# Optimization experiments

Hardware: AMD Instinct MI355X
Metric: run time of the kernel (lower is better)

Reference implementation:

```python
import jax, jax.numpy as jnp
import numpy as np

N, E, H, NH = 50000, 800000, 64, 4
DK = H // NH
EPS_LN = 1e-5


def _layernorm(h, g, b):
    mu = jnp.mean(h, axis=-1, keepdims=True)
    var = jnp.mean((h - mu) ** 2, axis=-1, keepdims=True)
    return (h - mu) * jax.lax.rsqrt(var + EPS_LN) * g + b


def _mlp(h, w0, b0, w1, b1, w2, b2, g, be):
    # Linear -> ReLU -> Linear -> ReLU -> Linear -> LayerNorm (mlp_layers=2)
    h = jax.nn.relu(h @ w0.T + b0)
    h = jax.nn.relu(h @ w1.T + b1)
    h = h @ w2.T + b2
    return _layernorm(h, g, be)


def setup_inputs() -> dict:
    key = jax.random.key(0)
    ks = jax.random.split(key, 24)
    s = lambda i, shape: jax.random.normal(ks[i], shape, jnp.float32) * (1.0 / np.sqrt(shape[-1]))
    inp = {
        "x": jax.random.normal(ks[0], (N, H), jnp.float32),
        "edge_index": jax.random.randint(ks[1], (2, E), 0, N),
        "edge_attr": jax.random.normal(ks[2], (E, H), jnp.float32),
        # edge MLP: Linear(3H,H), Linear(H,H), Linear(H,H), LayerNorm(H)
        "e_w0": s(3, (H, 3 * H)), "e_b0": jnp.zeros((H,)),
        "e_w1": s(4, (H, H)),     "e_b1": jnp.zeros((H,)),
        "e_w2": s(5, (H, H)),     "e_b2": jnp.zeros((H,)),
        "e_g": jnp.ones((H,)),    "e_be": jnp.zeros((H,)),
        # node MLP: Linear(2H,H), Linear(H,H), Linear(H,H), LayerNorm(H)
        "n_w0": s(6, (H, 2 * H)), "n_b0": jnp.zeros((H,)),
        "n_w1": s(7, (H, H)),     "n_b1": jnp.zeros((H,)),
        "n_w2": s(8, (H, H)),     "n_b2": jnp.zeros((H,)),
        "n_g": jnp.ones((H,)),    "n_be": jnp.zeros((H,)),
        "wq": s(9, (H, H)), "wk": s(10, (H, H)), "wv": s(11, (H, H)), "wo": s(12, (H, H)),
    }
    return inp


def reference(x, edge_index, edge_attr,
              e_w0, e_b0, e_w1, e_b1, e_w2, e_b2, e_g, e_be,
              n_w0, n_b0, n_w1, n_b1, n_w2, n_b2, n_g, n_be,
              wq, wk, wv, wo):
    src, dst = edge_index[0], edge_index[1]
    n_nodes, hid = x.shape
    n_edges = src.shape[0]
    x_dst, x_src = x[dst], x[src]  # [E,H] gathers

    e_new = _mlp(jnp.concatenate([x_dst, x_src, edge_attr], axis=-1),
                 e_w0, e_b0, e_w1, e_b1, e_w2, e_b2, e_g, e_be)

    Q = (x_dst @ wq.T).reshape(n_edges, NH, DK)
    K = (x_src @ wk.T).reshape(n_edges, NH, DK)
    V = (e_new @ wv.T).reshape(n_edges, NH, DK)

    scores = jnp.sum(Q * K, axis=-1) / np.sqrt(DK)  # [E,NH]
    smax = jax.ops.segment_max(scores, dst, num_segments=n_nodes)  # [N,NH]
    exp_s = jnp.exp(scores - smax[dst])
    sum_exp = jax.ops.segment_sum(exp_s, dst, num_segments=n_nodes)
    alpha = exp_s / (sum_exp[dst] + 1e-12)  # [E,NH]

    msg = jax.ops.segment_sum((alpha[..., None] * V).reshape(n_edges, hid),
                              dst, num_segments=n_nodes)  # [N,H]
    msg = msg @ wo.T

    x_new = x + _mlp(jnp.concatenate([x, msg], axis=-1),
                     n_w0, n_b0, n_w1, n_b1, n_w2, n_b2, n_g, n_be)
    return (x_new, edge_attr + e_new)
```

## Files before the change

kernel.cpp:

```cpp
#include <hip/hip_runtime.h>

typedef __bf16 bf16;
typedef __attribute__((ext_vector_type(8))) __bf16 bf16x8;
typedef __attribute__((ext_vector_type(4))) __bf16 bf16x4;
typedef __attribute__((ext_vector_type(4))) float  f32x4;

__device__ __forceinline__ f32x4 mfma16(bf16x8 a, bf16x8 b, f32x4 c) {
    return __builtin_amdgcn_mfma_f32_16x16x32_bf16(a, b, c, 0, 0, 0);
}

__device__ __forceinline__ void stash8(bf16* dst, float4 a, float4 b) {
    bf16x8 v;
    v[0] = (bf16)a.x; v[1] = (bf16)a.y; v[2] = (bf16)a.z; v[3] = (bf16)a.w;
    v[4] = (bf16)b.x; v[5] = (bf16)b.y; v[6] = (bf16)b.z; v[7] = (bf16)b.w;
    *reinterpret_cast<bf16x8*>(dst) = v;
}

__device__ __forceinline__ bf16x8 wfrag(const bf16* __restrict__ W, int s, int n, int lane) {
    return *reinterpret_cast<const bf16x8*>(W + (((s * 4 + n) * 64 + lane) * 8));
}

template<int P, int KS>
__device__ __forceinline__ void mm2s(const bf16* __restrict__ src, int kofs,
                                     const bf16* __restrict__ W,
                                     int lane, f32x4 (&acc)[2][4]) {
    const int c16 = lane & 15, g = lane >> 4;
#pragma unroll
    for (int m = 0; m < 2; ++m)
#pragma unroll
        for (int n = 0; n < 4; ++n) acc[m][n] = 0.0f;
#pragma unroll
    for (int s = 0; s < KS; ++s) {
        bf16x8 aA = *reinterpret_cast<const bf16x8*>(src + c16 * P + kofs + s * 32 + g * 8);
        bf16x8 aB = *reinterpret_cast<const bf16x8*>(src + (16 + c16) * P + kofs + s * 32 + g * 8);
#pragma unroll
        for (int n = 0; n < 4; ++n) {
            bf16x8 bb = wfrag(W, s, n, lane);
            acc[0][n] = mfma16(aA, bb, acc[0][n]);
            acc[1][n] = mfma16(aB, bb, acc[1][n]);
        }
    }
}

template<int P, int KS>
__device__ __forceinline__ void mm1s(const bf16* __restrict__ src, int kofs,
                                     const bf16* __restrict__ W,
                                     int lane, f32x4 (&acc)[4]) {
    const int c16 = lane & 15, g = lane >> 4;
#pragma unroll
    for (int n = 0; n < 4; ++n) acc[n] = 0.0f;
#pragma unroll
    for (int s = 0; s < KS; ++s) {
        bf16x8 a = *reinterpret_cast<const bf16x8*>(src + c16 * P + kofs + s * 32 + g * 8);
#pragma unroll
        for (int n = 0; n < 4; ++n) {
            bf16x8 bb = wfrag(W, s, n, lane);
            acc[n] = mfma16(a, bb, acc[n]);
        }
    }
}

__device__ __forceinline__ void storeh2(bf16* hbw, const f32x4 (&acc)[2][4],
                                        const float* __restrict__ bias, int c16, int g) {
#pragma unroll
    for (int n = 0; n < 4; ++n) {
        float bb = bias[n * 16 + c16];
#pragma unroll
        for (int m = 0; m < 2; ++m)
#pragma unroll
            for (int r = 0; r < 4; ++r)
                hbw[(m * 16 + g * 4 + r) * 72 + n * 16 + c16] = (bf16)fmaxf(acc[m][n][r] + bb, 0.0f);
    }
}

__device__ __forceinline__ void storeh1(bf16* hbw, const f32x4 (&acc)[4],
                                        const float* __restrict__ bias, int c16, int g) {
#pragma unroll
    for (int n = 0; n < 4; ++n) {
        float bb = bias[n * 16 + c16];
#pragma unroll
        for (int r = 0; r < 4; ++r)
            hbw[(g * 4 + r) * 72 + n * 16 + c16] = (bf16)fmaxf(acc[n][r] + bb, 0.0f);
    }
}

struct PrepArgs {
    const float* src[10];
    bf16* dst[10];
    int ofs[11];
    int ldk[10];
};

__global__ void prep_kernel(PrepArgs a, int totalFrag) {
    int t = blockIdx.x * 256 + threadIdx.x;
    if (t >= totalFrag) return;
    int eb = t * 8;
    int k = 0;
    while (k < 9 && eb >= a.ofs[k + 1]) ++k;
    int f = (eb - a.ofs[k]) >> 3;
    int lane = f & 63, n = (f >> 6) & 3, s = f >> 8;
    int c16 = lane & 15, g = lane >> 4;
    const float* sp = a.src[k] + (n * 16 + c16) * a.ldk[k] + s * 32 + g * 8;
    float4 v0 = *reinterpret_cast<const float4*>(sp);
    float4 v1 = *reinterpret_cast<const float4*>(sp + 4);
    stash8(a.dst[k] + (size_t)f * 8, v0, v1);
}

__global__ __launch_bounds__(256) void xb_kernel(const float* __restrict__ x,
                                                 bf16* __restrict__ xb, int total8) {
    int t = blockIdx.x * 256 + threadIdx.x;
    if (t >= total8) return;
    const float4* p = reinterpret_cast<const float4*>(x) + t * 2;
    stash8(xb + (size_t)t * 8, p[0], p[1]);
}

__global__ __launch_bounds__(256) void degcnt_kernel(const int* __restrict__ ei,
                                                     int* __restrict__ deg, int E) {
    int e = blockIdx.x * 256 + threadIdx.x;
    if (e < E) atomicAdd(&deg[ei[E + e]], 1);
}

__global__ __launch_bounds__(256) void scan1_kernel(const int* __restrict__ deg, int* __restrict__ ofs,
                                                    int* __restrict__ bsum, int N) {
    __shared__ int ws4[4];
    const int t = threadIdx.x, lane = t & 63, w = t >> 6;
    const int i = blockIdx.x * 256 + t;
    const int v = (i < N) ? deg[i] : 0;
    int inc = v;
#pragma unroll
    for (int o = 1; o < 64; o <<= 1) { int u = __shfl_up(inc, o); if (lane >= o) inc += u; }
    if (lane == 63) ws4[w] = inc;
    __syncthreads();
    int add = 0;
    for (int k = 0; k < w; ++k) add += ws4[k];
    if (i < N) ofs[i] = inc - v + add;
    if (t == 255) bsum[blockIdx.x] = inc + add;
}

__global__ __launch_bounds__(256) void scan2_kernel(int* __restrict__ bsum, int nb) {
    __shared__ int ws4[4];
    const int t = threadIdx.x, lane = t & 63, w = t >> 6;
    const int v = (t < nb) ? bsum[t] : 0;
    int inc = v;
#pragma unroll
    for (int o = 1; o < 64; o <<= 1) { int u = __shfl_up(inc, o); if (lane >= o) inc += u; }
    if (lane == 63) ws4[w] = inc;
    __syncthreads();
    int add = 0;
    for (int k = 0; k < w; ++k) add += ws4[k];
    if (t < nb) bsum[t] = inc - v + add;
}

__global__ __launch_bounds__(256) void scan3_kernel(int* __restrict__ ofs, const int* __restrict__ bsum, int N) {
    const int i = blockIdx.x * 256 + threadIdx.x;
    if (i < N) ofs[i] += bsum[blockIdx.x];
}

__global__ __launch_bounds__(256) void fill_kernel(const int* __restrict__ ei, const int* __restrict__ ofs,
                                                   int* __restrict__ cur, int* __restrict__ eidT, int E) {
    const int e = blockIdx.x * 256 + threadIdx.x;
    if (e >= E) return;
    const int d = ei[E + e];
    const int slot = atomicAdd(&cur[d], 1);
    eidT[ofs[d] + slot] = e;
}

__global__ __launch_bounds__(256, 4) void e1_kernel(
    const bf16* __restrict__ xb, const int* __restrict__ ei, const float* __restrict__ ea,
    const bf16* __restrict__ W0, const bf16* __restrict__ W1, const bf16* __restrict__ W2,
    const bf16* __restrict__ Wq, const bf16* __restrict__ Wk, const bf16* __restrict__ Wv,
    const float* __restrict__ b0, const float* __restrict__ b1, const float* __restrict__ b2,
    const float* __restrict__ egm, const float* __restrict__ ebe,
    float* __restrict__ scoresOut, bf16* __restrict__ Vout, float* __restrict__ eout, int E)
{
    __shared__ bf16 eas[4][32][72];
    __shared__ bf16 hbl[4][32][72];
    const int w = threadIdx.x >> 6;
    const int lane = threadIdx.x & 63;
    const int ebase = blockIdx.x * 128 + w * 32;
    bf16* eaw = &eas[w][0][0];
    bf16* hbw = &hbl[w][0][0];
    const int g = lane >> 4, c16 = lane & 15;

    {
        const int rr = lane >> 4;
        const int cc = (lane & 15) * 4;
#pragma unroll
        for (int i = 0; i < 8; ++i) {
            int row = i * 4 + rr;
            float4 v = *reinterpret_cast<const float4*>(ea + (size_t)(ebase + row) * 64 + cc);
            bf16x4 o;
            o[0] = (bf16)v.x; o[1] = (bf16)v.y; o[2] = (bf16)v.z; o[3] = (bf16)v.w;
            *reinterpret_cast<bf16x4*>(eaw + row * 72 + cc) = o;
        }
    }

    const int eA0 = ebase + c16, eA1 = ebase + 16 + c16;
    const int dn0 = ei[E + eA0], dn1 = ei[E + eA1];
    const int sn0 = ei[eA0],     sn1 = ei[eA1];
    const bf16* xd0 = xb + (size_t)dn0 * 64;
    const bf16* xd1 = xb + (size_t)dn1 * 64;
    const bf16* xs0 = xb + (size_t)sn0 * 64;
    const bf16* xs1 = xb + (size_t)sn1 * 64;
    bf16x8 fxd[2][2], fxs[2][2];
#pragma unroll
    for (int s = 0; s < 2; ++s) {
        fxd[0][s] = *reinterpret_cast<const bf16x8*>(xd0 + s * 32 + g * 8);
        fxd[1][s] = *reinterpret_cast<const bf16x8*>(xd1 + s * 32 + g * 8);
        fxs[0][s] = *reinterpret_cast<const bf16x8*>(xs0 + s * 32 + g * 8);
        fxs[1][s] = *reinterpret_cast<const bf16x8*>(xs1 + s * 32 + g * 8);
    }

    {
        f32x4 aq[2][4], ak[2][4];
#pragma unroll
        for (int m = 0; m < 2; ++m)
#pragma unroll
            for (int n = 0; n < 4; ++n) { aq[m][n] = 0.0f; ak[m][n] = 0.0f; }
#pragma unroll
        for (int s = 0; s < 2; ++s)
#pragma unroll
            for (int n = 0; n < 4; ++n) {
                bf16x8 bq = wfrag(Wq, s, n, lane);
                bf16x8 bk = wfrag(Wk, s, n, lane);
                aq[0][n] = mfma16(fxd[0][s], bq, aq[0][n]);
                aq[1][n] = mfma16(fxd[1][s], bq, aq[1][n]);
                ak[0][n] = mfma16(fxs[0][s], bk, ak[0][n]);
                ak[1][n] = mfma16(fxs[1][s], bk, ak[1][n]);
            }
        float* sst = reinterpret_cast<float*>(hbw);
#pragma unroll
        for (int n = 0; n < 4; ++n) {
#pragma unroll
            for (int m = 0; m < 2; ++m) {
                float pr[4];
#pragma unroll
                for (int r = 0; r < 4; ++r) pr[r] = aq[m][n][r] * ak[m][n][r];
#pragma unroll
                for (int ms = 1; ms < 16; ms <<= 1)
#pragma unroll
                    for (int r = 0; r < 4; ++r) pr[r] += __shfl_xor(pr[r], ms);
                if (c16 == n) {
#pragma unroll
                    for (int r = 0; r < 4; ++r)
                        sst[(m * 16 + g * 4 + r) * 4 + n] = pr[r] * 0.25f;
                }
            }
        }
        float2 sv = *reinterpret_cast<const float2*>(sst + lane * 2);
        *reinterpret_cast<float2*>(scoresOut + (size_t)ebase * 4 + lane * 2) = sv;
    }

    f32x4 acc[2][4], acc2[2][4];
#pragma unroll
    for (int m = 0; m < 2; ++m)
#pragma unroll
        for (int n = 0; n < 4; ++n) acc[m][n] = 0.0f;
#pragma unroll
    for (int s = 0; s < 2; ++s)
#pragma unroll
        for (int n = 0; n < 4; ++n) {
            bf16x8 bd = wfrag(W0, s, n, lane);
            acc[0][n] = mfma16(fxd[0][s], bd, acc[0][n]);
            acc[1][n] = mfma16(fxd[1][s], bd, acc[1][n]);
            bf16x8 bs = wfrag(W0, s + 2, n, lane);
            acc[0][n] = mfma16(fxs[0][s], bs, acc[0][n]);
            acc[1][n] = mfma16(fxs[1][s], bs, acc[1][n]);
        }
#pragma unroll
    for (int s = 0; s < 2; ++s) {
        bf16x8 ae0 = *reinterpret_cast<const bf16x8*>(eaw + c16 * 72 + s * 32 + g * 8);
        bf16x8 ae1 = *reinterpret_cast<const bf16x8*>(eaw + (16 + c16) * 72 + s * 32 + g * 8);
#pragma unroll
        for (int n = 0; n < 4; ++n) {
            bf16x8 be = wfrag(W0, s + 4, n, lane);
            acc[0][n] = mfma16(ae0, be, acc[0][n]);
            acc[1][n] = mfma16(ae1, be, acc[1][n]);
        }
    }

    storeh2(hbw, acc, b0, c16, g);
    mm2s<72, 2>(hbw, 0, W1, lane, acc);
    storeh2(hbw, acc, b1, c16, g);
    mm2s<72, 2>(hbw, 0, W2, lane, acc2);
#pragma unroll
    for (int n = 0; n < 4; ++n) {
        float bb = b2[n * 16 + c16];
#pragma unroll
        for (int m = 0; m < 2; ++m)
#pragma unroll
            for (int r = 0; r < 4; ++r) acc2[m][n][r] += bb;
    }

    float mu[2][4], rs[2][4];
#pragma unroll
    for (int m = 0; m < 2; ++m)
#pragma unroll
        for (int r = 0; r < 4; ++r) {
            float s1 = acc2[m][0][r] + acc2[m][1][r] + acc2[m][2][r] + acc2[m][3][r];
            for (int ms = 1; ms < 16; ms <<= 1) s1 += __shfl_xor(s1, ms);
            float mm = s1 * (1.0f / 64.0f);
            float d0 = acc2[m][0][r] - mm, d1 = acc2[m][1][r] - mm;
            float d2 = acc2[m][2][r] - mm, d3 = acc2[m][3][r] - mm;
            float sq = d0 * d0 + d1 * d1 + d2 * d2 + d3 * d3;
            for (int ms = 1; ms < 16; ms <<= 1) sq += __shfl_xor(sq, ms);
            mu[m][r] = mm;
            rs[m][r] = rsqrtf(sq * (1.0f / 64.0f) + 1e-5f);
        }

#pragma unroll
    for (int n = 0; n < 4; ++n) {
        float gg = egm[n * 16 + c16], bb = ebe[n * 16 + c16];
#pragma unroll
        for (int m = 0; m < 2; ++m)
#pragma unroll
            for (int r = 0; r < 4; ++r) {
                int rowi = m * 16 + g * 4 + r;
                float v = (acc2[m][n][r] - mu[m][r]) * rs[m][r] * gg + bb;
                hbw[rowi * 72 + n * 16 + c16] = (bf16)v;
            }
    }

    {
        const int rr = lane >> 4;
        const int cc = (lane & 15) * 4;
#pragma unroll
        for (int i = 0; i < 8; ++i) {
            int row = i * 4 + rr;
            bf16x4 hv = *reinterpret_cast<const bf16x4*>(hbw + row * 72 + cc);
            bf16x4 av = *reinterpret_cast<const bf16x4*>(eaw + row * 72 + cc);
            float4 o;
            o.x = (float)av[0] + (float)hv[0];
            o.y = (float)av[1] + (float)hv[1];
            o.z = (float)av[2] + (float)hv[2];
            o.w = (float)av[3] + (float)hv[3];
            *reinterpret_cast<float4*>(eout + (size_t)(ebase + row) * 64 + cc) = o;
        }
    }

    mm2s<72, 2>(hbw, 0, Wv, lane, acc);
#pragma unroll
    for (int n = 0; n < 4; ++n)
#pragma unroll
        for (int m = 0; m < 2; ++m)
#pragma unroll
            for (int r = 0; r < 4; ++r)
                eaw[(m * 16 + g * 4 + r) * 72 + n * 16 + c16] = (bf16)acc[m][n][r];
#pragma unroll
    for (int k = 0; k < 4; ++k) {
        int row = k * 8 + (lane >> 3);
        int col = (lane & 7) * 8;
        bf16x8 v = *reinterpret_cast<const bf16x8*>(eaw + row * 72 + col);
        *reinterpret_cast<bf16x8*>(Vout + (size_t)(ebase + row) * 64 + col) = v;
    }
}

__global__ __launch_bounds__(256) void gather_kernel(
    const int* __restrict__ deg, const int* __restrict__ ofs, const int* __restrict__ eidT,
    const float* __restrict__ scores, const bf16* __restrict__ V,
    bf16* __restrict__ msg, int N)
{
    const int w = threadIdx.x >> 6, lane = threadIdx.x & 63;
    const int n = blockIdx.x * 4 + w;
    if (n >= N) return;
    const int cnt = deg[n];
    const int* lst = eidT + ofs[n];
    const int h = lane >> 4;
    float m = -3.4e38f, s = 0.f, acc = 0.f;

    int eA = (lane < cnt) ? lst[lane] : 0;
    int eB = (64 + lane < cnt) ? lst[64 + lane] : 0;
    const int nr = min(cnt, 128);
    if (nr > 0) {
        int e = __shfl(eA, 0);
        float sc = scores[(size_t)e * 4 + h];
        float v  = (float)V[(size_t)e * 64 + lane];
        for (int i = 1; i <= nr; ++i) {
            float sc2 = 0.f, v2 = 0.f;
            if (i < nr) {
                int e2 = __shfl((i < 64) ? eA : eB, i & 63);
                sc2 = scores[(size_t)e2 * 4 + h];
                v2  = (float)V[(size_t)e2 * 64 + lane];
            }
            float mn = fmaxf(m, sc);
            float c  = __expf(m - mn);
            float ex = __expf(sc - mn);
            s = s * c + ex;
            acc = acc * c + ex * v;
            m = mn;
            sc = sc2; v = v2;
        }
    }
    for (int i = 128; i < cnt; ++i) {
        int e = lst[i];
        float sc = scores[(size_t)e * 4 + h];
        float v  = (float)V[(size_t)e * 64 + lane];
        float mn = fmaxf(m, sc);
        float c  = __expf(m - mn);
        float ex = __expf(sc - mn);
        s = s * c + ex;
        acc = acc * c + ex * v;
        m = mn;
    }
    msg[(size_t)n * 64 + lane] = (bf16)(acc / (s + 1e-12f));
}

__global__ __launch_bounds__(256, 4) void n_kernel(
    const float* __restrict__ x, const bf16* __restrict__ msg,
    const bf16* __restrict__ Wo, const bf16* __restrict__ W0, const bf16* __restrict__ W1,
    const bf16* __restrict__ W2,
    const float* __restrict__ b0, const float* __restrict__ b1, const float* __restrict__ b2,
    const float* __restrict__ ngm, const float* __restrict__ nbe,
    float* __restrict__ xout, int N)
{
    __shared__ bf16 cat[4][16][136];
    __shared__ bf16 hbl[4][16][72];
    const int w = threadIdx.x >> 6, lane = threadIdx.x & 63;
    const int nbase = blockIdx.x * 64 + w * 16;
    bf16* catw = &cat[w][0][0];
    bf16* hbw  = &hbl[w][0][0];

    {
        const int r = lane >> 2, q = lane & 3;
        const int nd = min(nbase + r, N - 1);
        const float4* xp = reinterpret_cast<const float4*>(x) + (size_t)nd * 16 + q * 4;
        stash8(catw + r * 136 + q * 16,     xp[0], xp[1]);
        stash8(catw + r * 136 + q * 16 + 8, xp[2], xp[3]);
        const bf16* mp = msg + (size_t)nd * 64 + q * 16;
        *reinterpret_cast<bf16x8*>(hbw + r * 72 + q * 16)     = *reinterpret_cast<const bf16x8*>(mp);
        *reinterpret_cast<bf16x8*>(hbw + r * 72 + q * 16 + 8) = *reinterpret_cast<const bf16x8*>(mp + 8);
    }
    const int g = lane >> 4, c16 = lane & 15;
    f32x4 acc[4];

    mm1s<72, 2>(hbw, 0, Wo, lane, acc);
#pragma unroll
    for (int n = 0; n < 4; ++n)
#pragma unroll
        for (int r = 0; r < 4; ++r)
            catw[(g * 4 + r) * 136 + 64 + n * 16 + c16] = (bf16)acc[n][r];

    mm1s<136, 4>(catw, 0, W0, lane, acc);
    storeh1(hbw, acc, b0, c16, g);
    mm1s<72, 2>(hbw, 0, W1, lane, acc);
    storeh1(hbw, acc, b1, c16, g);
    mm1s<72, 2>(hbw, 0, W2, lane, acc);
#pragma unroll
    for (int n = 0; n < 4; ++n) {
        float bb = b2[n * 16 + c16];
#pragma unroll
        for (int r = 0; r < 4; ++r) acc[n][r] += bb;
    }

    float mu[4], rs[4];
#pragma unroll
    for (int r = 0; r < 4; ++r) {
        float s1 = acc[0][r] + acc[1][r] + acc[2][r] + acc[3][r];
        for (int ms = 1; ms < 16; ms <<= 1) s1 += __shfl_xor(s1, ms);
        float mm = s1 * (1.0f / 64.0f);
        float d0 = acc[0][r] - mm, d1 = acc[1][r] - mm, d2 = acc[2][r] - mm, d3 = acc[3][r] - mm;
        float sq = d0 * d0 + d1 * d1 + d2 * d2 + d3 * d3;
        for (int ms = 1; ms < 16; ms <<= 1) sq += __shfl_xor(sq, ms);
        mu[r] = mm;
        rs[r] = rsqrtf(sq * (1.0f / 64.0f) + 1e-5f);
    }
#pragma unroll
    for (int n = 0; n < 4; ++n) {
        float gg = ngm[n * 16 + c16], bb = nbe[n * 16 + c16];
#pragma unroll
        for (int r = 0; r < 4; ++r) {
            int rowi = g * 4 + r;
            int node = nbase + rowi;
            float v = (acc[n][r] - mu[r]) * rs[r] * gg + bb;
            if (node < N) {
                size_t o = (size_t)node * 64 + n * 16 + c16;
                xout[o] = x[o] + v;
            }
        }
    }
}

extern "C" void kernel_launch(void* const* d_in, const int* in_sizes, int n_in,
                              void* d_out, int out_size, void* d_ws, size_t ws_size,
                              hipStream_t stream)
{
    const float* x   = (const float*)d_in[0];
    const int*   ei  = (const int*)d_in[1];
    const float* ea  = (const float*)d_in[2];
    const float* ew0 = (const float*)d_in[3];
    const float* eb0 = (const float*)d_in[4];
    const float* ew1 = (const float*)d_in[5];
    const float* eb1 = (const float*)d_in[6];
    const float* ew2 = (const float*)d_in[7];
    const float* eb2 = (const float*)d_in[8];
    const float* egm = (const float*)d_in[9];
    const float* ebe = (const float*)d_in[10];
    const float* nw0 = (const float*)d_in[11];
    const float* nb0 = (const float*)d_in[12];
    const float* nw1 = (const float*)d_in[13];
    const float* nb1 = (const float*)d_in[14];
    const float* nw2 = (const float*)d_in[15];
    const float* nb2 = (const float*)d_in[16];
    const float* ngm = (const float*)d_in[17];
    const float* nbe = (const float*)d_in[18];
    const float* wq  = (const float*)d_in[19];
    const float* wk  = (const float*)d_in[20];
    const float* wv  = (const float*)d_in[21];
    const float* wo  = (const float*)d_in[22];

    const int Nn = in_sizes[0] / 64;
    const int Ee = in_sizes[1] / 2;

    char* p = (char*)d_ws;
    auto carve = [&](size_t bytes) {
        char* r = p;
        p += (bytes + 255) & ~(size_t)255;
        return r;
    };
    bf16* W0e = (bf16*)carve(64 * 192 * 2);
    bf16* W1e = (bf16*)carve(64 * 64 * 2);
    bf16* W2e = (bf16*)carve(64 * 64 * 2);
    bf16* Wqb = (bf16*)carve(64 * 64 * 2);
    bf16* Wkb = (bf16*)carve(64 * 64 * 2);
    bf16* Wvb = (bf16*)carve(64 * 64 * 2);
    bf16* Wob = (bf16*)carve(64 * 64 * 2);
    bf16* W0n = (bf16*)carve(64 * 128 * 2);
    bf16* W1n = (bf16*)carve(64 * 64 * 2);
    bf16* W2n = (bf16*)carve(64 * 64 * 2);
    float* scores = (float*)carve((size_t)Ee * 4 * 4);
    bf16*  V      = (bf16*)carve((size_t)Ee * 64 * 2);
    bf16*  msg    = (bf16*)carve((size_t)Nn * 64 * 2);
    bf16*  xb     = (bf16*)carve((size_t)Nn * 64 * 2);
    int*   deg    = (int*)carve((size_t)Nn * 4);
    int*   ofs    = (int*)carve((size_t)Nn * 4);
    int*   cur    = (int*)carve((size_t)Nn * 4);
    int*   eidT   = (int*)carve((size_t)Ee * 4);
    int*   bsum   = (int*)carve(((size_t)Nn / 256 + 2) * 4);

    hipMemsetAsync(deg, 0, (size_t)Nn * 4, stream);
    hipMemsetAsync(cur, 0, (size_t)Nn * 4, stream);

    PrepArgs pa;
    const float* srcs[10] = {ew0, ew1, ew2, wq, wk, wv, wo, nw0, nw1, nw2};
    bf16* dsts[10]        = {W0e, W1e, W2e, Wqb, Wkb, Wvb, Wob, W0n, W1n, W2n};
    const int sizes[10]   = {12288, 4096, 4096, 4096, 4096, 4096, 4096, 8192, 4096, 4096};
    const int ldks[10]    = {192, 64, 64, 64, 64, 64, 64, 128, 64, 64};
    int acc_ofs = 0;
    for (int i = 0; i < 10; ++i) {
        pa.src[i] = srcs[i];
        pa.dst[i] = dsts[i];
        pa.ofs[i] = acc_ofs;
        pa.ldk[i] = ldks[i];
        acc_ofs += sizes[i];
    }
    pa.ofs[10] = acc_ofs;
    const int totalFrag = acc_ofs / 8;
    prep_kernel<<<(totalFrag + 255) / 256, 256, 0, stream>>>(pa, totalFrag);

    const int total8 = Nn * 64 / 8;
    xb_kernel<<<(total8 + 255) / 256, 256, 0, stream>>>(x, xb, total8);

    degcnt_kernel<<<(Ee + 255) / 256, 256, 0, stream>>>(ei, deg, Ee);
    const int nb = (Nn + 255) / 256;
    scan1_kernel<<<nb, 256, 0, stream>>>(deg, ofs, bsum, Nn);
    scan2_kernel<<<1, 256, 0, stream>>>(bsum, nb);
    scan3_kernel<<<nb, 256, 0, stream>>>(ofs, bsum, Nn);
    fill_kernel<<<(Ee + 255) / 256, 256, 0, stream>>>(ei, ofs, cur, eidT, Ee);

    float* xout = (float*)d_out;
    float* eout = (float*)d_out + (size_t)Nn * 64;

    e1_kernel<<<Ee / 128, 256, 0, stream>>>(xb, ei, ea,
                                            W0e, W1e, W2e, Wqb, Wkb, Wvb,
                                            eb0, eb1, eb2, egm, ebe,
                                            scores, V, eout, Ee);

    gather_kernel<<<(Nn + 3) / 4, 256, 0, stream>>>(deg, ofs, eidT, scores, V, msg, Nn);

    n_kernel<<<(Nn + 63) / 64, 256, 0, stream>>>(x, msg, Wob, W0n, W1n, W2n,
                                                 nb0, nb1, nb2, ngm, nbe, xout, Nn);
}
```

Measured before the change: 416.2 us.

## Loop e1 kernel over multiple tiles with software-prefetched gathers; fuse setup kernels

The edge kernel now processes five 128-edge tiles per block. While the current tile is computed, it prefetches the next tile's edge_attr, its edge indices and the gathered x rows into registers, to hide global gather latency behind the MFMA work. Launch bounds drop from 4 to 3 waves per SIMD to leave room for the extra registers, at some cost in occupancy. Separately, the weight prep, x-to-bf16 and degree-count kernels are merged into one launch to cut launch overhead.

```diff
diff --git a/kernel.cpp b/kernel.cpp
--- a/kernel.cpp
+++ b/kernel.cpp
@@ -91,33 +91,33 @@
     int ldk[10];
 };
 
-__global__ void prep_kernel(PrepArgs a, int totalFrag) {
+__global__ __launch_bounds__(256) void setup_kernel(PrepArgs a, int totalFrag,
+                                                    const float* __restrict__ x,
+                                                    bf16* __restrict__ xbuf, int total8,
+                                                    const int* __restrict__ ei,
+                                                    int* __restrict__ deg, int E) {
     int t = blockIdx.x * 256 + threadIdx.x;
-    if (t >= totalFrag) return;
-    int eb = t * 8;
-    int k = 0;
-    while (k < 9 && eb >= a.ofs[k + 1]) ++k;
-    int f = (eb - a.ofs[k]) >> 3;
-    int lane = f & 63, n = (f >> 6) & 3, s = f >> 8;
-    int c16 = lane & 15, g = lane >> 4;
-    const float* sp = a.src[k] + (n * 16 + c16) * a.ldk[k] + s * 32 + g * 8;
-    float4 v0 = *reinterpret_cast<const float4*>(sp);
-    float4 v1 = *reinterpret_cast<const float4*>(sp + 4);
-    stash8(a.dst[k] + (size_t)f * 8, v0, v1);
-}
-
-__global__ __launch_bounds__(256) void xb_kernel(const float* __restrict__ x,
-                                                 bf16* __restrict__ xb, int total8) {
-    int t = blockIdx.x * 256 + threadIdx.x;
-    if (t >= total8) return;
-    const float4* p = reinterpret_cast<const float4*>(x) + t * 2;
-    stash8(xb + (size_t)t * 8, p[0], p[1]);
-}
-
-__global__ __launch_bounds__(256) void degcnt_kernel(const int* __restrict__ ei,
-                                                     int* __restrict__ deg, int E) {
-    int e = blockIdx.x * 256 + threadIdx.x;
-    if (e < E) atomicAdd(&deg[ei[E + e]], 1);
+    if (t < totalFrag) {
+        int eb = t * 8;
+        int k = 0;
+        while (k < 9 && eb >= a.ofs[k + 1]) ++k;
+        int f = (eb - a.ofs[k]) >> 3;
+        int lane = f & 63, n = (f >> 6) & 3, s = f >> 8;
+        int c16 = lane & 15, g = lane >> 4;
+        const float* sp = a.src[k] + (n * 16 + c16) * a.ldk[k] + s * 32 + g * 8;
+        float4 v0 = *reinterpret_cast<const float4*>(sp);
+        float4 v1 = *reinterpret_cast<const float4*>(sp + 4);
+        stash8(a.dst[k] + (size_t)f * 8, v0, v1);
+        return;
+    }
+    t -= totalFrag;
+    if (t < total8) {
+        const float4* p = reinterpret_cast<const float4*>(x) + t * 2;
+        stash8(xbuf + (size_t)t * 8, p[0], p[1]);
+        return;
+    }
+    t -= total8;
+    if (t < E) atomicAdd(&deg[ei[E + t]], 1);
 }
 
 __global__ __launch_bounds__(256) void scan1_kernel(const int* __restrict__ deg, int* __restrict__ ofs,
@@ -165,165 +165,187 @@
     eidT[ofs[d] + slot] = e;
 }
 
-__global__ __launch_bounds__(256, 4) void e1_kernel(
+template<int T>
+__global__ __launch_bounds__(256, 3) void e1_kernel(
     const bf16* __restrict__ xb, const int* __restrict__ ei, const float* __restrict__ ea,
     const bf16* __restrict__ W0, const bf16* __restrict__ W1, const bf16* __restrict__ W2,
     const bf16* __restrict__ Wq, const bf16* __restrict__ Wk, const bf16* __restrict__ Wv,
     const float* __restrict__ b0, const float* __restrict__ b1, const float* __restrict__ b2,
     const float* __restrict__ egm, const float* __restrict__ ebe,
-    float* __restrict__ scoresOut, bf16* __restrict__ Vout, float* __restrict__ eout, int E)
+    float* __restrict__ scoresOut, bf16* __restrict__ Vout, float* __restrict__ eout,
+    int tileOfs, int E)
 {
     __shared__ bf16 eas[4][32][72];
     __shared__ bf16 hbl[4][32][72];
     const int w = threadIdx.x >> 6;
     const int lane = threadIdx.x & 63;
-    const int ebase = blockIdx.x * 128 + w * 32;
+    const int g = lane >> 4, c16 = lane & 15;
+    const int rr = lane >> 4, cc = (lane & 15) * 4;
     bf16* eaw = &eas[w][0][0];
     bf16* hbw = &hbl[w][0][0];
-    const int g = lane >> 4, c16 = lane & 15;
-
+    const int tile0 = tileOfs + blockIdx.x * T;
+
+    float4 eaP[8];
+    int dn0, dn1, sn0, sn1;
     {
-        const int rr = lane >> 4;
-        const int cc = (lane & 15) * 4;
+        const int tb = tile0 * 128 + w * 32;
+#pragma unroll
+        for (int i = 0; i < 8; ++i)
+            eaP[i] = *reinterpret_cast<const float4*>(ea + (size_t)(tb + i * 4 + rr) * 64 + cc);
+        dn0 = ei[E + tb + c16]; dn1 = ei[E + tb + 16 + c16];
+        sn0 = ei[tb + c16];     sn1 = ei[tb + 16 + c16];
+    }
+    bf16x8 fxd[2][2], fxs[2][2];
+#pragma unroll
+    for (int s = 0; s < 2; ++s) {
+        fxd[0][s] = *reinterpret_cast<const bf16x8*>(xb + (size_t)dn0 * 64 + s * 32 + g * 8);
+        fxd[1][s] = *reinterpret_cast<const bf16x8*>(xb + (size_t)dn1 * 64 + s * 32 + g * 8);
+        fxs[0][s] = *reinterpret_cast<const bf16x8*>(xb + (size_t)sn0 * 64 + s * 32 + g * 8);
+        fxs[1][s] = *reinterpret_cast<const bf16x8*>(xb + (size_t)sn1 * 64 + s * 32 + g * 8);
+    }
+
+    for (int k = 0; k < T; ++k) {
+        const int ebase = (tile0 + k) * 128 + w * 32;
+
 #pragma unroll
         for (int i = 0; i < 8; ++i) {
-            int row = i * 4 + rr;
-            float4 v = *reinterpret_cast<const float4*>(ea + (size_t)(ebase + row) * 64 + cc);
             bf16x4 o;
-            o[0] = (bf16)v.x; o[1] = (bf16)v.y; o[2] = (bf16)v.z; o[3] = (bf16)v.w;
-            *reinterpret_cast<bf16x4*>(eaw + row * 72 + cc) = o;
-        }
-    }
-
-    const int eA0 = ebase + c16, eA1 = ebase + 16 + c16;
-    const int dn0 = ei[E + eA0], dn1 = ei[E + eA1];
-    const int sn0 = ei[eA0],     sn1 = ei[eA1];
-    const bf16* xd0 = xb + (size_t)dn0 * 64;
-    const bf16* xd1 = xb + (size_t)dn1 * 64;
-    const bf16* xs0 = xb + (size_t)sn0 * 64;
-    const bf16* xs1 = xb + (size_t)sn1 * 64;
-    bf16x8 fxd[2][2], fxs[2][2];
-#pragma unroll
-    for (int s = 0; s < 2; ++s) {
-        fxd[0][s] = *reinterpret_cast<const bf16x8*>(xd0 + s * 32 + g * 8);
-        fxd[1][s] = *reinterpret_cast<const bf16x8*>(xd1 + s * 32 + g * 8);
-        fxs[0][s] = *reinterpret_cast<const bf16x8*>(xs0 + s * 32 + g * 8);
-        fxs[1][s] = *reinterpret_cast<const bf16x8*>(xs1 + s * 32 + g * 8);
-    }
-
-    {
-        f32x4 aq[2][4], ak[2][4];
+            o[0] = (bf16)eaP[i].x; o[1] = (bf16)eaP[i].y;
+            o[2] = (bf16)eaP[i].z; o[3] = (bf16)eaP[i].w;
+            *reinterpret_cast<bf16x4*>(eaw + (i * 4 + rr) * 72 + cc) = o;
+        }
+
+        int ndn0, ndn1, nsn0, nsn1;
+        if (k + 1 < T) {
+            const int nb = ebase + 128;
+#pragma unroll
+            for (int i = 0; i < 8; ++i)
+                eaP[i] = *reinterpret_cast<const float4*>(ea + (size_t)(nb + i * 4 + rr) * 64 + cc);
+            ndn0 = ei[E + nb + c16]; ndn1 = ei[E + nb + 16 + c16];
+            nsn0 = ei[nb + c16];     nsn1 = ei[nb + 16 + c16];
+        }
+
+        {
+            f32x4 aq[2][4], ak[2][4];
+#pragma unroll
+            for (int m = 0; m < 2; ++m)
+#pragma unroll
+                for (int n = 0; n < 4; ++n) { aq[m][n] = 0.0f; ak[m][n] = 0.0f; }
+#pragma unroll
+            for (int s = 0; s < 2; ++s)
+#pragma unroll
+                for (int n = 0; n < 4; ++n) {
+                    bf16x8 bq = wfrag(Wq, s, n, lane);
+                    bf16x8 bk = wfrag(Wk, s, n, lane);
+                    aq[0][n] = mfma16(fxd[0][s], bq, aq[0][n]);
+                    aq[1][n] = mfma16(fxd[1][s], bq, aq[1][n]);
+                    ak[0][n] = mfma16(fxs[0][s], bk, ak[0][n]);
+                    ak[1][n] = mfma16(fxs[1][s], bk, ak[1][n]);
+                }
+            float* sst = reinterpret_cast<float*>(hbw);
+#pragma unroll
+            for (int n = 0; n < 4; ++n) {
+#pragma unroll
+                for (int m = 0; m < 2; ++m) {
+                    float pr[4];
+#pragma unroll
+                    for (int r = 0; r < 4; ++r) pr[r] = aq[m][n][r] * ak[m][n][r];
+#pragma unroll
+                    for (int ms = 1; ms < 16; ms <<= 1)
+#pragma unroll
+                        for (int r = 0; r < 4; ++r) pr[r] += __shfl_xor(pr[r], ms);
+                    if (c16 == n) {
+#pragma unroll
+                        for (int r = 0; r < 4; ++r)
+                            sst[(m * 16 + g * 4 + r) * 4 + n] = pr[r] * 0.25f;
+                    }
+                }
+            }
+            float2 sv = *reinterpret_cast<const float2*>(sst + lane * 2);
+            *reinterpret_cast<float2*>(scoresOut + (size_t)ebase * 4 + lane * 2) = sv;
+        }
+
+        f32x4 acc[2][4], acc2[2][4];
 #pragma unroll
         for (int m = 0; m < 2; ++m)
 #pragma unroll
-            for (int n = 0; n < 4; ++n) { aq[m][n] = 0.0f; ak[m][n] = 0.0f; }
+            for (int n = 0; n < 4; ++n) acc[m][n] = 0.0f;
 #pragma unroll
         for (int s = 0; s < 2; ++s)
 #pragma unroll
             for (int n = 0; n < 4; ++n) {
-                bf16x8 bq = wfrag(Wq, s, n, lane);
-                bf16x8 bk = wfrag(Wk, s, n, lane);
-                aq[0][n] = mfma16(fxd[0][s], bq, aq[0][n]);
-                aq[1][n] = mfma16(fxd[1][s], bq, aq[1][n]);
-                ak[0][n] = mfma16(fxs[0][s], bk, ak[0][n]);
-                ak[1][n] = mfma16(fxs[1][s], bk, ak[1][n]);
-            }
-        float* sst = reinterpret_cast<float*>(hbw);
+                bf16x8 bd = wfrag(W0, s, n, lane);
+                acc[0][n] = mfma16(fxd[0][s], bd, acc[0][n]);
+                acc[1][n] = mfma16(fxd[1][s], bd, acc[1][n]);
+                bf16x8 bs = wfrag(W0, s + 2, n, lane);
+                acc[0][n] = mfma16(fxs[0][s], bs, acc[0][n]);
+                acc[1][n] = mfma16(fxs[1][s], bs, acc[1][n]);
+            }
+#pragma unroll
+        for (int s = 0; s < 2; ++s) {
+            bf16x8 ae0 = *reinterpret_cast<const bf16x8*>(eaw + c16 * 72 + s * 32 + g * 8);
+            bf16x8 ae1 = *reinterpret_cast<const bf16x8*>(eaw + (16 + c16) * 72 + s * 32 + g * 8);
+#pragma unroll
+            for (int n = 0; n < 4; ++n) {
+                bf16x8 be = wfrag(W0, s + 4, n, lane);
+                acc[0][n] = mfma16(ae0, be, acc[0][n]);
+                acc[1][n] = mfma16(ae1, be, acc[1][n]);
+            }
+        }
+
+        bf16x8 nfxd[2][2], nfxs[2][2];
+        if (k + 1 < T) {
+#pragma unroll
+            for (int s = 0; s < 2; ++s) {
+                nfxd[0][s] = *reinterpret_cast<const bf16x8*>(xb + (size_t)ndn0 * 64 + s * 32 + g * 8);
+                nfxd[1][s] = *reinterpret_cast<const bf16x8*>(xb + (size_t)ndn1 * 64 + s * 32 + g * 8);
+                nfxs[0][s] = *reinterpret_cast<const bf16x8*>(xb + (size_t)nsn0 * 64 + s * 32 + g * 8);
+                nfxs[1][s] = *reinterpret_cast<const bf16x8*>(xb + (size_t)nsn1 * 64 + s * 32 + g * 8);
+            }
+        }
+
+        storeh2(hbw, acc, b0, c16, g);
+        mm2s<72, 2>(hbw, 0, W1, lane, acc);
+        storeh2(hbw, acc, b1, c16, g);
+        mm2s<72, 2>(hbw, 0, W2, lane, acc2);
 #pragma unroll
         for (int n = 0; n < 4; ++n) {
-#pragma unroll
-            for (int m = 0; m < 2; ++m) {
-                float pr[4];
-#pragma unroll
-                for (int r = 0; r < 4; ++r) pr[r] = aq[m][n][r] * ak[m][n][r];
-#pragma unroll
-                for (int ms = 1; ms < 16; ms <<= 1)
-#pragma unroll
-                    for (int r = 0; r < 4; ++r) pr[r] += __shfl_xor(pr[r], ms);
-                if (c16 == n) {
-#pragma unroll
-                    for (int r = 0; r < 4; ++r)
-                        sst[(m * 16 + g * 4 + r) * 4 + n] = pr[r] * 0.25f;
+            float bb = b2[n * 16 + c16];
+#pragma unroll
+            for (int m = 0; m < 2; ++m)
+#pragma unroll
+                for (int r = 0; r < 4; ++r) acc2[m][n][r] += bb;
+        }
+
+        float mu[2][4], rs[2][4];
+#pragma unroll
+        for (int m = 0; m < 2; ++m)
+#pragma unroll
+            for (int r = 0; r < 4; ++r) {
+                float s1 = acc2[m][0][r] + acc2[m][1][r] + acc2[m][2][r] + acc2[m][3][r];
+                for (int ms = 1; ms < 16; ms <<= 1) s1 += __shfl_xor(s1, ms);
+                float mm = s1 * (1.0f / 64.0f);
+                float d0 = acc2[m][0][r] - mm, d1 = acc2[m][1][r] - mm;
+                float d2 = acc2[m][2][r] - mm, d3 = acc2[m][3][r] - mm;
+                float sq = d0 * d0 + d1 * d1 + d2 * d2 + d3 * d3;
+                for (int ms = 1; ms < 16; ms <<= 1) sq += __shfl_xor(sq, ms);
+                mu[m][r] = mm;
+                rs[m][r] = rsqrtf(sq * (1.0f / 64.0f) + 1e-5f);
+            }
+
+#pragma unroll
+        for (int n = 0; n < 4; ++n) {
+            float gg = egm[n * 16 + c16], bb = ebe[n * 16 + c16];
+#pragma unroll
+            for (int m = 0; m < 2; ++m)
+#pragma unroll
+                for (int r = 0; r < 4; ++r) {
+                    int rowi = m * 16 + g * 4 + r;
+                    float v = (acc2[m][n][r] - mu[m][r]) * rs[m][r] * gg + bb;
+                    hbw[rowi * 72 + n * 16 + c16] = (bf16)v;
                 }
-            }
-        }
-        float2 sv = *reinterpret_cast<const float2*>(sst + lane * 2);
-        *reinterpret_cast<float2*>(scoresOut + (size_t)ebase * 4 + lane * 2) = sv;
-    }
-
-    f32x4 acc[2][4], acc2[2][4];
-#pragma unroll
-    for (int m = 0; m < 2; ++m)
-#pragma unroll
-        for (int n = 0; n < 4; ++n) acc[m][n] = 0.0f;
-#pragma unroll
-    for (int s = 0; s < 2; ++s)
-#pragma unroll
-        for (int n = 0; n < 4; ++n) {
-            bf16x8 bd = wfrag(W0, s, n, lane);
-            acc[0][n] = mfma16(fxd[0][s], bd, acc[0][n]);
-            acc[1][n] = mfma16(fxd[1][s], bd, acc[1][n]);
-            bf16x8 bs = wfrag(W0, s + 2, n, lane);
-            acc[0][n] = mfma16(fxs[0][s], bs, acc[0][n]);
-            acc[1][n] = mfma16(fxs[1][s], bs, acc[1][n]);
-        }
-#pragma unroll
-    for (int s = 0; s < 2; ++s) {
-        bf16x8 ae0 = *reinterpret_cast<const bf16x8*>(eaw + c16 * 72 + s * 32 + g * 8);
-        bf16x8 ae1 = *reinterpret_cast<const bf16x8*>(eaw + (16 + c16) * 72 + s * 32 + g * 8);
-#pragma unroll
-        for (int n = 0; n < 4; ++n) {
-            bf16x8 be = wfrag(W0, s + 4, n, lane);
-            acc[0][n] = mfma16(ae0, be, acc[0][n]);
-            acc[1][n] = mfma16(ae1, be, acc[1][n]);
-        }
-    }
-
-    storeh2(hbw, acc, b0, c16, g);
-    mm2s<72, 2>(hbw, 0, W1, lane, acc);
-    storeh2(hbw, acc, b1, c16, g);
-    mm2s<72, 2>(hbw, 0, W2, lane, acc2);
-#pragma unroll
-    for (int n = 0; n < 4; ++n) {
-        float bb = b2[n * 16 + c16];
-#pragma unroll
-        for (int m = 0; m < 2; ++m)
-#pragma unroll
-            for (int r = 0; r < 4; ++r) acc2[m][n][r] += bb;
-    }
-
-    float mu[2][4], rs[2][4];
-#pragma unroll
-    for (int m = 0; m < 2; ++m)
-#pragma unroll
-        for (int r = 0; r < 4; ++r) {
-            float s1 = acc2[m][0][r] + acc2[m][1][r] + acc2[m][2][r] + acc2[m][3][r];
-            for (int ms = 1; ms < 16; ms <<= 1) s1 += __shfl_xor(s1, ms);
-            float mm = s1 * (1.0f / 64.0f);
-            float d0 = acc2[m][0][r] - mm, d1 = acc2[m][1][r] - mm;
-            float d2 = acc2[m][2][r] - mm, d3 = acc2[m][3][r] - mm;
-            float sq = d0 * d0 + d1 * d1 + d2 * d2 + d3 * d3;
-            for (int ms = 1; ms < 16; ms <<= 1) sq += __shfl_xor(sq, ms);
-            mu[m][r] = mm;
-            rs[m][r] = rsqrtf(sq * (1.0f / 64.0f) + 1e-5f);
-        }
-
-#pragma unroll
-    for (int n = 0; n < 4; ++n) {
-        float gg = egm[n * 16 + c16], bb = ebe[n * 16 + c16];
-#pragma unroll
-        for (int m = 0; m < 2; ++m)
-#pragma unroll
-            for (int r = 0; r < 4; ++r) {
-                int rowi = m * 16 + g * 4 + r;
-                float v = (acc2[m][n][r] - mu[m][r]) * rs[m][r] * gg + bb;
-                hbw[rowi * 72 + n * 16 + c16] = (bf16)v;
-            }
-    }
-
-    {
-        const int rr = lane >> 4;
-        const int cc = (lane & 15) * 4;
+        }
+
 #pragma unroll
         for (int i = 0; i < 8; ++i) {
             int row = i * 4 + rr;
@@ -336,22 +358,31 @@
             o.w = (float)av[3] + (float)hv[3];
             *reinterpret_cast<float4*>(eout + (size_t)(ebase + row) * 64 + cc) = o;
         }
-    }
-
-    mm2s<72, 2>(hbw, 0, Wv, lane, acc);
-#pragma unroll
-    for (int n = 0; n < 4; ++n)
-#pragma unroll
-        for (int m = 0; m < 2; ++m)
-#pragma unroll
-            for (int r = 0; r < 4; ++r)
-                eaw[(m * 16 + g * 4 + r) * 72 + n * 16 + c16] = (bf16)acc[m][n][r];
-#pragma unroll
-    for (int k = 0; k < 4; ++k) {
-        int row = k * 8 + (lane >> 3);
-        int col = (lane & 7) * 8;
-        bf16x8 v = *reinterpret_cast<const bf16x8*>(eaw + row * 72 + col);
-        *reinterpret_cast<bf16x8*>(Vout + (size_t)(ebase + row) * 64 + col) = v;
+
+        mm2s<72, 2>(hbw, 0, Wv, lane, acc);
+#pragma unroll
+        for (int n = 0; n < 4; ++n)
+#pragma unroll
+            for (int m = 0; m < 2; ++m)
+#pragma unroll
+                for (int r = 0; r < 4; ++r)
+                    eaw[(m * 16 + g * 4 + r) * 72 + n * 16 + c16] = (bf16)acc[m][n][r];
+#pragma unroll
+        for (int kk = 0; kk < 4; ++kk) {
+            int row = kk * 8 + (lane >> 3);
+            int col = (lane & 7) * 8;
+            bf16x8 v = *reinterpret_cast<const bf16x8*>(eaw + row * 72 + col);
+            *reinterpret_cast<bf16x8*>(Vout + (size_t)(ebase + row) * 64 + col) = v;
+        }
+
+        if (k + 1 < T) {
+#pragma unroll
+            for (int s = 0; s < 2; ++s) {
+                fxd[0][s] = nfxd[0][s]; fxd[1][s] = nfxd[1][s];
+                fxs[0][s] = nfxs[0][s]; fxs[1][s] = nfxs[1][s];
+            }
+            dn0 = ndn0; dn1 = ndn1; sn0 = nsn0; sn1 = nsn1;
+        }
     }
 }
 
@@ -555,12 +586,11 @@
     }
     pa.ofs[10] = acc_ofs;
     const int totalFrag = acc_ofs / 8;
-    prep_kernel<<<(totalFrag + 255) / 256, 256, 0, stream>>>(pa, totalFrag);
-
     const int total8 = Nn * 64 / 8;
-    xb_kernel<<<(total8 + 255) / 256, 256, 0, stream>>>(x, xb, total8);
-
-    degcnt_kernel<<<(Ee + 255) / 256, 256, 0, stream>>>(ei, deg, Ee);
+    const int setupTotal = totalFrag + total8 + Ee;
+    setup_kernel<<<(setupTotal + 255) / 256, 256, 0, stream>>>(pa, totalFrag, x, xb, total8,
+                                                               ei, deg, Ee);
+
     const int nb = (Nn + 255) / 256;
     scan1_kernel<<<nb, 256, 0, stream>>>(deg, ofs, bsum, Nn);
     scan2_kernel<<<1, 256, 0, stream>>>(bsum, nb);
@@ -570,10 +600,18 @@
     float* xout = (float*)d_out;
     float* eout = (float*)d_out + (size_t)Nn * 64;
 
-    e1_kernel<<<Ee / 128, 256, 0, stream>>>(xb, ei, ea,
-                                            W0e, W1e, W2e, Wqb, Wkb, Wvb,
-                                            eb0, eb1, eb2, egm, ebe,
-                                            scores, V, eout, Ee);
+    const int tiles = Ee / 128;
+    const int TT = 5;
+    const int NB = tiles / TT;
+    const int rem = tiles - NB * TT;
+    if (NB > 0)
+        e1_kernel<5><<<NB, 256, 0, stream>>>(xb, ei, ea, W0e, W1e, W2e, Wqb, Wkb, Wvb,
+                                             eb0, eb1, eb2, egm, ebe,
+                                             scores, V, eout, 0, Ee);
+    if (rem > 0)
+        e1_kernel<1><<<rem, 256, 0, stream>>>(xb, ei, ea, W0e, W1e, W2e, Wqb, Wkb, Wvb,
+                                              eb0, eb1, eb2, egm, ebe,
+                                              scores, V, eout, NB * TT, Ee);
 
     gather_kernel<<<(Nn + 3) / 4, 256, 0, stream>>>(deg, ofs, eidT, scores, V, msg, Nn);
 
```

Result: slower. 964.6 us (+131.8%).

## Merge setup kernels, fold cur reset into scan, store scores as bf16

Applied to the files above, without the earlier changes.

Fuses the weight-prep, x-to-bf16 and degree-count kernels into one launch. The cur counter is now zeroed inside scan3 instead of by a separate memset. Attention scores are stored and read as bf16 instead of fp32, which halves that intermediate's traffic. Together these cut launch overhead and some memory traffic, at the cost of lower score precision before the softmax.

```diff
diff --git a/kernel.cpp b/kernel.cpp
--- a/kernel.cpp
+++ b/kernel.cpp
@@ -3,6 +3,7 @@
 typedef __bf16 bf16;
 typedef __attribute__((ext_vector_type(8))) __bf16 bf16x8;
 typedef __attribute__((ext_vector_type(4))) __bf16 bf16x4;
+typedef __attribute__((ext_vector_type(2))) __bf16 bf16x2;
 typedef __attribute__((ext_vector_type(4))) float  f32x4;
 
 __device__ __forceinline__ f32x4 mfma16(bf16x8 a, bf16x8 b, f32x4 c) {
@@ -91,33 +92,33 @@
     int ldk[10];
 };
 
-__global__ void prep_kernel(PrepArgs a, int totalFrag) {
+__global__ __launch_bounds__(256) void setup_kernel(PrepArgs a, int totalFrag,
+                                                    const float* __restrict__ x,
+                                                    bf16* __restrict__ xbuf, int total8,
+                                                    const int* __restrict__ ei,
+                                                    int* __restrict__ deg, int E) {
     int t = blockIdx.x * 256 + threadIdx.x;
-    if (t >= totalFrag) return;
-    int eb = t * 8;
-    int k = 0;
-    while (k < 9 && eb >= a.ofs[k + 1]) ++k;
-    int f = (eb - a.ofs[k]) >> 3;
-    int lane = f & 63, n = (f >> 6) & 3, s = f >> 8;
-    int c16 = lane & 15, g = lane >> 4;
-    const float* sp = a.src[k] + (n * 16 + c16) * a.ldk[k] + s * 32 + g * 8;
-    float4 v0 = *reinterpret_cast<const float4*>(sp);
-    float4 v1 = *reinterpret_cast<const float4*>(sp + 4);
-    stash8(a.dst[k] + (size_t)f * 8, v0, v1);
-}
-
-__global__ __launch_bounds__(256) void xb_kernel(const float* __restrict__ x,
-                                                 bf16* __restrict__ xb, int total8) {
-    int t = blockIdx.x * 256 + threadIdx.x;
-    if (t >= total8) return;
-    const float4* p = reinterpret_cast<const float4*>(x) + t * 2;
-    stash8(xb + (size_t)t * 8, p[0], p[1]);
-}
-
-__global__ __launch_bounds__(256) void degcnt_kernel(const int* __restrict__ ei,
-                                                     int* __restrict__ deg, int E) {
-    int e = blockIdx.x * 256 + threadIdx.x;
-    if (e < E) atomicAdd(&deg[ei[E + e]], 1);
+    if (t < totalFrag) {
+        int eb = t * 8;
+        int k = 0;
+        while (k < 9 && eb >= a.ofs[k + 1]) ++k;
+        int f = (eb - a.ofs[k]) >> 3;
+        int lane = f & 63, n = (f >> 6) & 3, s = f >> 8;
+        int c16 = lane & 15, g = lane >> 4;
+        const float* sp = a.src[k] + (n * 16 + c16) * a.ldk[k] + s * 32 + g * 8;
+        float4 v0 = *reinterpret_cast<const float4*>(sp);
+        float4 v1 = *reinterpret_cast<const float4*>(sp + 4);
+        stash8(a.dst[k] + (size_t)f * 8, v0, v1);
+        return;
+    }
+    t -= totalFrag;
+    if (t < total8) {
+        const float4* p = reinterpret_cast<const float4*>(x) + t * 2;
+        stash8(xbuf + (size_t)t * 8, p[0], p[1]);
+        return;
+    }
+    t -= total8;
+    if (t < E) atomicAdd(&deg[ei[E + t]], 1);
 }
 
 __global__ __launch_bounds__(256) void scan1_kernel(const int* __restrict__ deg, int* __restrict__ ofs,
@@ -151,9 +152,13 @@
     if (t < nb) bsum[t] = inc - v + add;
 }
 
-__global__ __launch_bounds__(256) void scan3_kernel(int* __restrict__ ofs, const int* __restrict__ bsum, int N) {
+__global__ __launch_bounds__(256) void scan3_kernel(int* __restrict__ ofs, const int* __restrict__ bsum,
+                                                    int* __restrict__ cur, int N) {
     const int i = blockIdx.x * 256 + threadIdx.x;
-    if (i < N) ofs[i] += bsum[blockIdx.x];
+    if (i < N) {
+        ofs[i] += bsum[blockIdx.x];
+        cur[i] = 0;
+    }
 }
 
 __global__ __launch_bounds__(256) void fill_kernel(const int* __restrict__ ei, const int* __restrict__ ofs,
@@ -171,7 +176,7 @@
     const bf16* __restrict__ Wq, const bf16* __restrict__ Wk, const bf16* __restrict__ Wv,
     const float* __restrict__ b0, const float* __restrict__ b1, const float* __restrict__ b2,
     const float* __restrict__ egm, const float* __restrict__ ebe,
-    float* __restrict__ scoresOut, bf16* __restrict__ Vout, float* __restrict__ eout, int E)
+    bf16* __restrict__ scoresOut, bf16* __restrict__ Vout, float* __restrict__ eout, int E)
 {
     __shared__ bf16 eas[4][32][72];
     __shared__ bf16 hbl[4][32][72];
@@ -248,7 +253,9 @@
             }
         }
         float2 sv = *reinterpret_cast<const float2*>(sst + lane * 2);
-        *reinterpret_cast<float2*>(scoresOut + (size_t)ebase * 4 + lane * 2) = sv;
+        bf16x2 so;
+        so[0] = (bf16)sv.x; so[1] = (bf16)sv.y;
+        *reinterpret_cast<bf16x2*>(scoresOut + (size_t)ebase * 4 + lane * 2) = so;
     }
 
     f32x4 acc[2][4], acc2[2][4];
@@ -357,7 +364,7 @@
 
 __global__ __launch_bounds__(256) void gather_kernel(
     const int* __restrict__ deg, const int* __restrict__ ofs, const int* __restrict__ eidT,
-    const float* __restrict__ scores, const bf16* __restrict__ V,
+    const bf16* __restrict__ scores, const bf16* __restrict__ V,
     bf16* __restrict__ msg, int N)
 {
     const int w = threadIdx.x >> 6, lane = threadIdx.x & 63;
@@ -373,13 +380,13 @@
     const int nr = min(cnt, 128);
     if (nr > 0) {
         int e = __shfl(eA, 0);
-        float sc = scores[(size_t)e * 4 + h];
+        float sc = (float)scores[(size_t)e * 4 + h];
         float v  = (float)V[(size_t)e * 64 + lane];
         for (int i = 1; i <= nr; ++i) {
             float sc2 = 0.f, v2 = 0.f;
             if (i < nr) {
                 int e2 = __shfl((i < 64) ? eA : eB, i & 63);
-                sc2 = scores[(size_t)e2 * 4 + h];
+                sc2 = (float)scores[(size_t)e2 * 4 + h];
                 v2  = (float)V[(size_t)e2 * 64 + lane];
             }
             float mn = fmaxf(m, sc);
@@ -393,7 +400,7 @@
     }
     for (int i = 128; i < cnt; ++i) {
         int e = lst[i];
-        float sc = scores[(size_t)e * 4 + h];
+        float sc = (float)scores[(size_t)e * 4 + h];
         float v  = (float)V[(size_t)e * 64 + lane];
         float mn = fmaxf(m, sc);
         float c  = __expf(m - mn);
@@ -527,7 +534,7 @@
     bf16* W0n = (bf16*)carve(64 * 128 * 2);
     bf16* W1n = (bf16*)carve(64 * 64 * 2);
     bf16* W2n = (bf16*)carve(64 * 64 * 2);
-    float* scores = (float*)carve((size_t)Ee * 4 * 4);
+    bf16*  scores = (bf16*)carve((size_t)Ee * 4 * 2);
     bf16*  V      = (bf16*)carve((size_t)Ee * 64 * 2);
     bf16*  msg    = (bf16*)carve((size_t)Nn * 64 * 2);
     bf16*  xb     = (bf16*)carve((size_t)Nn * 64 * 2);
@@ -538,7 +545,6 @@
     int*   bsum   = (int*)carve(((size_t)Nn / 256 + 2) * 4);
 
     hipMemsetAsync(deg, 0, (size_t)Nn * 4, stream);
-    hipMemsetAsync(cur, 0, (size_t)Nn * 4, stream);
 
     PrepArgs pa;
     const float* srcs[10] = {ew0, ew1, ew2, wq, wk, wv, wo, nw0, nw1, nw2};
@@ -555,16 +561,15 @@
     }
     pa.ofs[10] = acc_ofs;
     const int totalFrag = acc_ofs / 8;
-    prep_kernel<<<(totalFrag + 255) / 256, 256, 0, stream>>>(pa, totalFrag);
-
     const int total8 = Nn * 64 / 8;
-    xb_kernel<<<(total8 + 255) / 256, 256, 0, stream>>>(x, xb, total8);
-
-    degcnt_kernel<<<(Ee + 255) / 256, 256, 0, stream>>>(ei, deg, Ee);
+    const int setupTotal = totalFrag + total8 + Ee;
+    setup_kernel<<<(setupTotal + 255) / 256, 256, 0, stream>>>(pa, totalFrag, x, xb, total8,
+                                                               ei, deg, Ee);
+
     const int nb = (Nn + 255) / 256;
     scan1_kernel<<<nb, 256, 0, stream>>>(deg, ofs, bsum, Nn);
     scan2_kernel<<<1, 256, 0, stream>>>(bsum, nb);
-    scan3_kernel<<<nb, 256, 0, stream>>>(ofs, bsum, Nn);
+    scan3_kernel<<<nb, 256, 0, stream>>>(ofs, bsum, cur, Nn);
     fill_kernel<<<(Ee + 255) / 256, 256, 0, stream>>>(ei, ofs, cur, eidT, Ee);
 
     float* xout = (float*)d_out;
```

After: 396.5 us. 1.05x faster.
